# Kernel optimization log

Measured on AMD Instinct MI355X. Metric: run time of the kernel, lower is better.

## Reference

```python
import jax, jax.numpy as jnp
import numpy as np

B, S, HID = 1, 2048, 4096
NH, NKV, HD = 32, 8, 128
N_REP = NH // NKV
EPS = 1e-5
ROPE_THETA = 500000.0


def setup_inputs() -> dict:
    key = jax.random.key(0)
    ks = jax.random.split(key, 16)
    s = 0.02
    return {
        "hidden_states": jax.random.normal(ks[0], (B, S, HID), jnp.float32),
        "Wq": jax.random.normal(ks[1], (NH * HD, HID), jnp.float32) * s,
        "bq": jnp.zeros((NH * HD,), jnp.float32),
        "Wk": jax.random.normal(ks[2], (NKV * HD, HID), jnp.float32) * s,
        "bk": jnp.zeros((NKV * HD,), jnp.float32),
        "Wv": jax.random.normal(ks[3], (NKV * HD, HID), jnp.float32) * s,
        "bv": jnp.zeros((NKV * HD,), jnp.float32),
        "Wo": jax.random.normal(ks[4], (HID, HID), jnp.float32) * s,
        "bo": jnp.zeros((HID,), jnp.float32),
        "qn_g": jnp.ones((HD,), jnp.float32),
        "qn_b": jnp.zeros((HD,), jnp.float32),
        "kn_g": jnp.ones((HD,), jnp.float32),
        "kn_b": jnp.zeros((HD,), jnp.float32),
    }


def _layernorm(x, g, b):
    mu = jnp.mean(x, axis=-1, keepdims=True)
    var = jnp.var(x, axis=-1, keepdims=True)
    return (x - mu) * jax.lax.rsqrt(var + EPS) * g + b


def _rope_tables(seq_len, dtype):
    inv_freq = 1.0 / ROPE_THETA ** (jnp.arange(0, HD, 2, dtype=jnp.float32) / HD)
    pos = jnp.arange(seq_len, dtype=jnp.float32)
    freqs = pos[:, None] * inv_freq[None, :]          # (S, HD/2)
    emb = jnp.concatenate([freqs, freqs], axis=-1)    # (S, HD)
    return jnp.cos(emb).astype(dtype), jnp.sin(emb).astype(dtype)


def _rotate_half(x):
    x1, x2 = x[..., : HD // 2], x[..., HD // 2 :]
    return jnp.concatenate([-x2, x1], axis=-1)


def reference(hidden_states, Wq, bq, Wk, bk, Wv, bv, Wo, bo, qn_g, qn_b, kn_g, kn_b):
    x = hidden_states
    q = (x @ Wq.T + bq).reshape(B, S, NH, HD)
    k = (x @ Wk.T + bk).reshape(B, S, NKV, HD)
    v = (x @ Wv.T + bv).reshape(B, S, NKV, HD)
    # QK-Norm (LayerNorm over head_dim)
    q = _layernorm(q, qn_g, qn_b).transpose(0, 2, 1, 3)  # (B, NH, S, HD)
    k = _layernorm(k, kn_g, kn_b).transpose(0, 2, 1, 3)  # (B, NKV, S, HD)
    v = v.transpose(0, 2, 1, 3)
    # RoPE
    cos, sin = _rope_tables(S, x.dtype)  # (S, HD) each, broadcast over B, heads
    q = q * cos + _rotate_half(q) * sin
    k = k * cos + _rotate_half(k) * sin
    # GQA: repeat KV heads
    k = jnp.repeat(k, N_REP, axis=1)  # (B, NH, S, HD)
    v = jnp.repeat(v, N_REP, axis=1)
    # Causal attention
    scores = jnp.einsum("bhqd,bhkd->bhqk", q, k) / jnp.sqrt(jnp.float32(HD)).astype(x.dtype)
    causal = jnp.tril(jnp.ones((S, S), bool))
    scores = jnp.where(causal, scores, jnp.finfo(scores.dtype).min)
    attn = jax.nn.softmax(scores, axis=-1)
    out = jnp.einsum("bhqk,bhkd->bhqd", attn, v)
    out = out.transpose(0, 2, 1, 3).reshape(B, S, HID)
    return out @ Wo.T + bo
```

## Files before the change

kernel.cpp:

```cpp
#include <hip/hip_runtime.h>

typedef __bf16 bf16;
typedef __bf16 bf16x8 __attribute__((ext_vector_type(8)));
typedef __bf16 bf16x4 __attribute__((ext_vector_type(4)));
typedef float f32x4 __attribute__((ext_vector_type(4)));

#define S_LEN 2048
#define HID 4096
#define NH 32
#define NKV 8
#define HD 128
#define QSTR 6144
#define SCALE 0.08838834764831845f
#define QSCL 0.1275164918918885f
#define M2C 16.33f

template <int V> struct IC { static constexpr int value = V; };

__device__ __forceinline__ bf16x8 load8(const bf16* p) { return *(const bf16x8*)p; }
__device__ __forceinline__ bf16x8 load8(const float* p) {
    float4 a = *(const float4*)p;
    float4 b = *(const float4*)(p + 4);
    bf16x8 r;
    r[0] = (bf16)a.x; r[1] = (bf16)a.y; r[2] = (bf16)a.z; r[3] = (bf16)a.w;
    r[4] = (bf16)b.x; r[5] = (bf16)b.y; r[6] = (bf16)b.z; r[7] = (bf16)b.w;
    return r;
}

__device__ __forceinline__ void load_lds16(const bf16* g, bf16* l) {
    __builtin_amdgcn_global_load_lds(
        (const __attribute__((address_space(1))) void*)g,
        (__attribute__((address_space(3))) void*)l, 16, 0, 0);
}

template <int C> __device__ __forceinline__ void vmwait_if() {
    if constexpr (C >= 0) asm volatile("s_waitcnt vmcnt(%0)" ::"n"(C) : "memory");
}

__device__ __forceinline__ void lgkm0() {
    asm volatile("s_waitcnt lgkmcnt(0)" ::: "memory");
    __builtin_amdgcn_sched_barrier(0);
}

__global__ __launch_bounds__(256) void cvt5(const float* __restrict__ x,
                                            const float* __restrict__ Wq,
                                            const float* __restrict__ Wk,
                                            const float* __restrict__ Wv,
                                            const float* __restrict__ Wo,
                                            bf16* __restrict__ xb,
                                            bf16* __restrict__ Wqkv,
                                            bf16* __restrict__ Wob) {
    int i = blockIdx.x * 256 + threadIdx.x;
    const float* src;
    bf16* dst;
    if (i < 1048576)      { src = x  + (size_t)i * 8;              dst = xb + (size_t)i * 8; }
    else if (i < 3145728) { size_t j = i - 1048576; src = Wq + j * 8; dst = Wqkv + j * 8; }
    else if (i < 3670016) { size_t j = i - 3145728; src = Wk + j * 8; dst = Wqkv + 16777216 + j * 8; }
    else if (i < 4194304) { size_t j = i - 3670016; src = Wv + j * 8; dst = Wqkv + 20971520 + j * 8; }
    else                  { size_t j = i - 4194304; src = Wo + j * 8; dst = Wob + j * 8; }
    *(bf16x8*)dst = load8(src);
}

template <int BM, int BN, int WM, int WN, int BMODE, typename TO>
__global__ __launch_bounds__(512, 2) void gemm8(const bf16* __restrict__ A,
                                                const bf16* __restrict__ Bw,
                                                const float* __restrict__ b0,
                                                const float* __restrict__ b1,
                                                const float* __restrict__ b2,
                                                TO* __restrict__ out,
                                                int N, int K) {
    constexpr int RW  = BM / WM;
    constexpr int CW  = BN / WN;
    constexpr int FM  = RW / 16;
    constexpr int FN  = CW / 16;
    constexpr int FMH = FM / 2;
    constexpr int FNH0 = (FN + 1) / 2, FNH1 = FN - FNH0;
    constexpr int SZ0 = FNH0 * 16, SZ1 = FNH1 * 16;
    constexpr int AROWS_H = BM / 2;
    constexpr int B0ROWS = WN * SZ0, B1ROWS = WN * SZ1;
    constexpr int LA  = AROWS_H / 64;
    constexpr int LB0 = B0ROWS / 64, LB1 = B1ROWS / 64;
    constexpr int V0  = 2 * LA + LB0;
    constexpr int V3  = 2 * LA + LB0 + LB1;
    constexpr int V3T = LA + LB1;

    __shared__ __align__(16) bf16 AS[2 * BM * 64];
    __shared__ __align__(16) bf16 BS[2 * BN * 64];

    const int tid  = threadIdx.x;
    const int wave = tid >> 6;
    const int lane = tid & 63;
    const int quad = lane >> 4;
    const int l16  = lane & 15;
    const int wm   = wave / WN;
    const int wn   = wave % WN;

    const int gx   = gridDim.x;
    const int nwg  = gx * gridDim.y;
    const int orig = blockIdx.y * gx + blockIdx.x;
    int wg = orig;
    if ((nwg & 7) == 0) wg = (orig & 7) * (nwg >> 3) + (orig >> 3);
    const int row0 = (wg / gx) * BM;
    const int col0 = (wg % gx) * BN;

    auto stageA = [&](int mh, int bufv, int kt) {
#pragma unroll
        for (int j = 0; j < LA; ++j) {
            int c = j * 512 + tid;
            int r = c >> 3, pg = c & 7;
            int g = pg ^ (r & 7);
            int gr = (r / (RW / 2)) * RW + mh * (RW / 2) + (r % (RW / 2));
            load_lds16(&A[(size_t)(row0 + gr) * K + kt * 64 + g * 8],
                       &AS[bufv * (BM * 64) + mh * (AROWS_H * 64) + c * 8]);
        }
    };
    auto stageB0 = [&](int bufv, int kt) {
#pragma unroll
        for (int j = 0; j < LB0; ++j) {
            int c = j * 512 + tid;
            int r = c >> 3, pg = c & 7;
            int g = pg ^ (r & 7);
            int gc = (r / SZ0) * CW + (r % SZ0);
            load_lds16(&Bw[(size_t)(col0 + gc) * K + kt * 64 + g * 8],
                       &BS[bufv * (BN * 64) + c * 8]);
        }
    };
    auto stageB1 = [&](int bufv, int kt) {
#pragma unroll
        for (int j = 0; j < LB1; ++j) {
            int c = j * 512 + tid;
            int r = c >> 3, pg = c & 7;
            int g = pg ^ (r & 7);
            int gc = (r / SZ1) * CW + SZ0 + (r % SZ1);
            load_lds16(&Bw[(size_t)(col0 + gc) * K + kt * 64 + g * 8],
                       &BS[bufv * (BN * 64) + B0ROWS * 64 + c * 8]);
        }
    };

    f32x4 acc[FM][FN];
#pragma unroll
    for (int mi = 0; mi < FM; ++mi)
#pragma unroll
        for (int ni = 0; ni < FN; ++ni) { f32x4 z = {0.f, 0.f, 0.f, 0.f}; acc[mi][ni] = z; }

    bf16x8 af[FMH][2];
    bf16x8 bfv[FN][2];

    auto loadA = [&](int mh, int bufv) {
#pragma unroll
        for (int mi = 0; mi < FMH; ++mi)
#pragma unroll
            for (int ks = 0; ks < 2; ++ks) {
                int r = wm * (RW / 2) + mi * 16 + l16;
                int g = ks * 4 + quad;
                af[mi][ks] = *(const bf16x8*)&AS[bufv * (BM * 64) + mh * (AROWS_H * 64) +
                                                 r * 64 + ((g ^ (r & 7)) << 3)];
            }
    };
    auto loadB = [&](auto cNH, int bufv) {
        constexpr int NHv = decltype(cNH)::value;
        constexpr int CNT = NHv ? FNH1 : FNH0;
        constexpr int SZ  = NHv ? SZ1 : SZ0;
#pragma unroll
        for (int nj = 0; nj < CNT; ++nj)
#pragma unroll
            for (int ks = 0; ks < 2; ++ks) {
                int r = wn * SZ + nj * 16 + l16;
                int g = ks * 4 + quad;
                bfv[NHv * FNH0 + nj][ks] =
                    *(const bf16x8*)&BS[bufv * (BN * 64) + NHv * (B0ROWS * 64) +
                                        r * 64 + ((g ^ (r & 7)) << 3)];
            }
    };
    auto mmac = [&](auto cMH, auto cNH) {
        constexpr int MH = decltype(cMH)::value, NHv = decltype(cNH)::value;
        constexpr int NB = NHv ? FNH0 : 0, NE = NHv ? FN : FNH0;
        __builtin_amdgcn_s_setprio(1);
#pragma unroll
        for (int mi = 0; mi < FMH; ++mi)
#pragma unroll
            for (int ni = NB; ni < NE; ++ni)
#pragma unroll
                for (int ks = 0; ks < 2; ++ks)
                    acc[MH * FMH + mi][ni] = __builtin_amdgcn_mfma_f32_16x16x32_bf16(
                        af[mi][ks], bfv[ni][ks], acc[MH * FMH + mi][ni], 0, 0, 0);
        __builtin_amdgcn_s_setprio(0);
    };

    auto run_tile = [&](int t, auto cSA1, auto cSB1, auto cSA0, auto cSB0,
                        auto cV0, auto cV3) {
        const int buf = t & 1, nbuf = buf ^ 1;
        loadA(0, buf);
        loadB(IC<0>{}, buf);
        if constexpr (decltype(cSA1)::value) stageA(1, nbuf, t + 1);
        __builtin_amdgcn_s_barrier();
        lgkm0();
        mmac(IC<0>{}, IC<0>{});
        vmwait_if<decltype(cV0)::value>();
        __builtin_amdgcn_s_barrier();
        loadB(IC<1>{}, buf);
        if constexpr (decltype(cSB1)::value) stageB1(nbuf, t + 1);
        __builtin_amdgcn_s_barrier();
        lgkm0();
        mmac(IC<0>{}, IC<1>{});
        __builtin_amdgcn_s_barrier();
        loadA(1, buf);
        if constexpr (decltype(cSA0)::value) stageA(0, buf, t + 2);
        __builtin_amdgcn_s_barrier();
        lgkm0();
        mmac(IC<1>{}, IC<0>{});
        __builtin_amdgcn_s_barrier();
        if constexpr (decltype(cSB0)::value) stageB0(buf, t + 2);
        __builtin_amdgcn_s_barrier();
        lgkm0();
        mmac(IC<1>{}, IC<1>{});
        vmwait_if<decltype(cV3)::value>();
        __builtin_amdgcn_s_barrier();
    };

    stageA(0, 0, 0); stageB0(0, 0);
    stageA(1, 0, 0); stageB1(0, 0);
    stageA(0, 1, 1); stageB0(1, 1);
    vmwait_if<V3>();
    __builtin_amdgcn_s_barrier();

    const int NT = K >> 6;
    for (int t = 0; t < NT - 2; ++t)
        run_tile(t, IC<1>{}, IC<1>{}, IC<1>{}, IC<1>{}, IC<V0>{}, IC<V3>{});
    run_tile(NT - 2, IC<1>{}, IC<1>{}, IC<0>{}, IC<0>{}, IC<V0>{}, IC<V3T>{});
    run_tile(NT - 1, IC<0>{}, IC<0>{}, IC<0>{}, IC<0>{}, IC<0>{}, IC<-1>{});

#pragma unroll
    for (int ni = 0; ni < FN; ++ni) {
        int n = col0 + wn * CW + ni * 16 + l16;
        float bv;
        if (BMODE == 0) bv = b0[n];
        else bv = (n < 4096) ? b0[n] : ((n < 5120) ? b1[n - 4096] : b2[n - 5120]);
#pragma unroll
        for (int mi = 0; mi < FM; ++mi) {
            int m = row0 + wm * RW + mi * 16 + quad * 4;
#pragma unroll
            for (int reg = 0; reg < 4; ++reg)
                out[(size_t)(m + reg) * N + n] = (TO)(acc[mi][ni][reg] + bv);
        }
    }
}

__global__ __launch_bounds__(256) void ln_rope(bf16* __restrict__ qkv,
                                               const float* __restrict__ qg, const float* __restrict__ qbt,
                                               const float* __restrict__ kg, const float* __restrict__ kbt) {
    int row  = blockIdx.x * 4 + (threadIdx.x >> 6);
    int lane = threadIdx.x & 63;

    bf16* ptr;
    const float *g, *bb;
    int s;
    float osc;
    if (row < S_LEN * NH) {
        s   = row >> 5;
        ptr = qkv + (size_t)s * QSTR + (row & 31) * HD;
        g   = qg; bb = qbt; osc = QSCL;
    } else {
        int r2 = row - S_LEN * NH;
        s   = r2 >> 3;
        ptr = qkv + (size_t)s * QSTR + 4096 + (r2 & 7) * HD;
        g   = kg; bb = kbt; osc = 1.f;
    }

    float x1 = (float)ptr[lane];
    float x2 = (float)ptr[lane + 64];
    float sum = x1 + x2;
    float sq  = x1 * x1 + x2 * x2;
#pragma unroll
    for (int m = 1; m < 64; m <<= 1) {
        sum += __shfl_xor(sum, m);
        sq  += __shfl_xor(sq, m);
    }
    float mu  = sum * (1.f / 128.f);
    float var = sq * (1.f / 128.f) - mu * mu;
    float rs  = rsqrtf(var + 1e-5f);
    float n1  = (x1 - mu) * rs * g[lane] + bb[lane];
    float n2  = (x2 - mu) * rs * g[lane + 64] + bb[lane + 64];

    float inv = exp2f(-0.2958057514f * (float)lane);
    float ang = (float)s * inv;
    float sn, cs;
    sincosf(ang, &sn, &cs);

    ptr[lane]      = (bf16)((n1 * cs - n2 * sn) * osc);
    ptr[lane + 64] = (bf16)((n2 * cs + n1 * sn) * osc);
}

__global__ __launch_bounds__(256) void transpose_v(const bf16* __restrict__ qkv,
                                                   bf16* __restrict__ vT) {
    __shared__ bf16 Ts[64 * 64];
    const int c0 = blockIdx.x * 64;
    const int s0 = blockIdx.y * 64;
    const int tid = threadIdx.x;

#pragma unroll
    for (int i = 0; i < 2; ++i) {
        int cc = i * 256 + tid;
        int r = cc >> 3, col8 = cc & 7;
        *(bf16x8*)&Ts[r * 64 + ((col8 ^ (r & 7)) << 3)] =
            *(const bf16x8*)&qkv[(size_t)(s0 + r) * QSTR + 5120 + c0 + (col8 << 3)];
    }
    __syncthreads();
#pragma unroll
    for (int i = 0; i < 2; ++i) {
        int oc = i * 256 + tid;
        int c = oc & 63, sb = oc >> 6;
        bf16x8 r8;
#pragma unroll
        for (int j = 0; j < 8; ++j) {
            int sg = sb * 8 + j;
            r8[j] = Ts[sg * 64 + ((((c >> 3) ^ (sg & 7)) << 3) + (c & 7))];
        }
        *(bf16x8*)&vT[(size_t)(c0 + c) * S_LEN + s0 + sb * 8] = r8;
    }
}

__global__ __launch_bounds__(512) void attn6(const bf16* __restrict__ qkv,
                                             const bf16* __restrict__ vT,
                                             bf16* __restrict__ abuf) {
    const int pairp = blockIdx.x;
    const int kvh   = blockIdx.y;
    const int tid   = threadIdx.x;
    const int wave  = tid >> 6;
    const int lane  = tid & 63;
    const int quad  = lane >> 4;
    const int l16   = lane & 15;
    const int spw   = wave >> 2;
    const int hw    = wave & 3;
    const int h     = kvh * 4 + hw;

    __shared__ __align__(16) bf16 smem[4 * 8192 + 2 * 8192 + 8 * 2048];
    bf16* Ksb = smem;
    bf16* Vtb = smem + 4 * 8192;
    bf16* Psb = smem + 6 * 8192;

    bf16x8 onesf;
#pragma unroll
    for (int j = 0; j < 8; ++j) onesf[j] = (bf16)1.f;

    auto stageK = [&](int pr, int kb) {
#pragma unroll
        for (int j = 0; j < 4; ++j) {
            int c = j * 512 + tid;
            int tile = c >> 10, cc = c & 1023;
            int key = cc >> 4, pg = cc & 15;
            int g = pg ^ (key & 7);
            load_lds16(&qkv[(size_t)((2 * pr + tile) * 64 + key) * QSTR + 4096 +
                            kvh * HD + g * 8],
                       &Ksb[(kb * 2 + tile) * 8192 + cc * 8]);
        }
    };
    auto stageV = [&](int pr) {
#pragma unroll
        for (int j = 0; j < 4; ++j) {
            int c = j * 512 + tid;
            int tile = c >> 10, cc = c & 1023;
            int d = cc >> 3, pg = cc & 7;
            int g = pg ^ (d & 7);
            load_lds16(&vT[(size_t)(kvh * HD + d) * S_LEN + (2 * pr + tile) * 64 + g * 8],
                       &Vtb[tile * 8192 + cc * 8]);
        }
    };

    for (int ph = 0; ph < 2; ++ph) {
        const int qt  = ph ? (63 - pairp) : pairp;
        const int r0  = qt * 32;
        const int nkt = qt / 2 + 1;
        const int nit = (nkt + 1) >> 1;

        bf16x8 qf[2][4];
#pragma unroll
        for (int mi = 0; mi < 2; ++mi)
#pragma unroll
            for (int ks = 0; ks < 4; ++ks)
                qf[mi][ks] = *(const bf16x8*)&qkv[(size_t)(r0 + mi * 16 + l16) * QSTR +
                                                  h * HD + ks * 32 + quad * 8];

        f32x4 o_acc[2][8];
#pragma unroll
        for (int mi = 0; mi < 2; ++mi)
#pragma unroll
            for (int ni = 0; ni < 8; ++ni) {
                f32x4 z = {0.f, 0.f, 0.f, 0.f};
                o_acc[mi][ni] = z;
            }
        f32x4 lacc[2];
#pragma unroll
        for (int mi = 0; mi < 2; ++mi) { f32x4 z = {0.f, 0.f, 0.f, 0.f}; lacc[mi] = z; }

        stageK(0, 0);

        for (int it = 0; it < nit; ++it) {
            const int kb = it & 1;
            stageV(it);
            if (it + 1 < nit) { stageK(it + 1, kb ^ 1); vmwait_if<8>(); }
            else              { vmwait_if<4>(); }
            __syncthreads();

            const int kt = 2 * it + spw;
            const bf16* Kw = Ksb + (kb * 2 + spw) * 8192;
            const bf16* Vw = Vtb + spw * 8192;
            bf16* Pw = Psb + wave * 2048;

            if (kt < nkt) {
                f32x4 sacc[2][4];
#pragma unroll
                for (int mi = 0; mi < 2; ++mi)
#pragma unroll
                    for (int ni = 0; ni < 4; ++ni) {
                        f32x4 z = {0.f, 0.f, 0.f, 0.f};
                        sacc[mi][ni] = z;
                    }
                __builtin_amdgcn_s_setprio(1);
#pragma unroll
                for (int ks = 0; ks < 4; ++ks)
#pragma unroll
                    for (int ni = 0; ni < 4; ++ni) {
                        bf16x8 kf = *(const bf16x8*)&Kw[(ni * 16 + l16) * 128 +
                                                        ((((ks << 2) + quad) ^ (l16 & 7)) << 3)];
                        sacc[0][ni] = __builtin_amdgcn_mfma_f32_16x16x32_bf16(qf[0][ks], kf, sacc[0][ni], 0, 0, 0);
                        sacc[1][ni] = __builtin_amdgcn_mfma_f32_16x16x32_bf16(qf[1][ks], kf, sacc[1][ni], 0, 0, 0);
                    }
                __builtin_amdgcn_s_setprio(0);

#pragma unroll
                for (int mi = 0; mi < 2; ++mi)
#pragma unroll
                    for (int reg = 0; reg < 4; ++reg) {
                        int rloc = mi * 16 + quad * 4 + reg;
                        int qrow = r0 + rloc;
#pragma unroll
                        for (int ni = 0; ni < 4; ++ni) {
                            int key = kt * 64 + ni * 16 + l16;
                            float t = (key > qrow) ? -1e30f : (sacc[mi][ni][reg] - M2C);
                            float p = exp2f(t);
                            int blk = (ni * 2 + (l16 >> 3)) ^ (rloc & 7);
                            Pw[rloc * 64 + blk * 8 + (l16 & 7)] = (bf16)p;
                        }
                    }
            }

            if (it + 1 < nit) vmwait_if<4>();
            else              vmwait_if<0>();
            __syncthreads();

            if (kt < nkt) {
                const bf16* Vw2 = Vw;
                bf16* Pw2 = Pw;
                __builtin_amdgcn_s_setprio(1);
#pragma unroll
                for (int ks2 = 0; ks2 < 2; ++ks2) {
                    bf16x8 pa[2];
#pragma unroll
                    for (int mi = 0; mi < 2; ++mi) {
                        int rloc = mi * 16 + l16;
                        pa[mi] = *(const bf16x8*)&Pw2[rloc * 64 +
                                                      ((((ks2 << 2) + quad) ^ (rloc & 7)) << 3)];
                    }
#pragma unroll
                    for (int ni = 0; ni < 8; ++ni) {
                        int d = ni * 16 + l16;
                        bf16x8 vf = *(const bf16x8*)&Vw2[d * 64 + ((((ks2 << 2) + quad) ^ (d & 7)) << 3)];
                        o_acc[0][ni] = __builtin_amdgcn_mfma_f32_16x16x32_bf16(pa[0], vf, o_acc[0][ni], 0, 0, 0);
                        o_acc[1][ni] = __builtin_amdgcn_mfma_f32_16x16x32_bf16(pa[1], vf, o_acc[1][ni], 0, 0, 0);
                    }
                    lacc[0] = __builtin_amdgcn_mfma_f32_16x16x32_bf16(pa[0], onesf, lacc[0], 0, 0, 0);
                    lacc[1] = __builtin_amdgcn_mfma_f32_16x16x32_bf16(pa[1], onesf, lacc[1], 0, 0, 0);
                }
                __builtin_amdgcn_s_setprio(0);
            }
            __syncthreads();
        }

        float* M  = (float*)smem;
        float* Ls = (float*)&smem[4 * 8192];
        if (spw == 1) {
            float* Mw = M + hw * 4096;
#pragma unroll
            for (int mi = 0; mi < 2; ++mi)
#pragma unroll
                for (int ni = 0; ni < 8; ++ni)
#pragma unroll
                    for (int j = 0; j < 4; ++j)
                        Mw[((mi * 8 + ni) * 4 + j) * 64 + lane] = o_acc[mi][ni][j];
            if (l16 == 0)
#pragma unroll
                for (int mi = 0; mi < 2; ++mi)
#pragma unroll
                    for (int reg = 0; reg < 4; ++reg)
                        Ls[hw * 32 + mi * 16 + quad * 4 + reg] = lacc[mi][reg];
        }
        __syncthreads();
        if (spw == 0) {
            float* Mw = M + hw * 4096;
#pragma unroll
            for (int mi = 0; mi < 2; ++mi) {
                float linv[4];
#pragma unroll
                for (int reg = 0; reg < 4; ++reg)
                    linv[reg] = 1.f / fmaxf(lacc[mi][reg] +
                                            Ls[hw * 32 + mi * 16 + quad * 4 + reg], 1e-30f);
#pragma unroll
                for (int ni = 0; ni < 8; ++ni)
#pragma unroll
                    for (int reg = 0; reg < 4; ++reg) {
                        float v = o_acc[mi][ni][reg] + Mw[((mi * 8 + ni) * 4 + reg) * 64 + lane];
                        int s = r0 + mi * 16 + quad * 4 + reg;
                        abuf[(size_t)s * HID + h * HD + ni * 16 + l16] = (bf16)(v * linv[reg]);
                    }
            }
        }
        __syncthreads();
    }
}

template <typename TA, typename TO>
__global__ __launch_bounds__(256) void gemm_bt(const TA* __restrict__ A,
                                               const float* __restrict__ W,
                                               const float* __restrict__ bias,
                                               TO* __restrict__ out,
                                               int N, int K) {
    __shared__ __align__(16) bf16 As[128 * 64];
    __shared__ __align__(16) bf16 Bs[128 * 64];
    const int tid = threadIdx.x, wave = tid >> 6, lane = tid & 63;
    const int quad = lane >> 4, l16 = lane & 15, wm = wave >> 1, wn = wave & 1;
    const int row0 = blockIdx.y * 128, col0 = blockIdx.x * 128;
    f32x4 acc[4][4];
#pragma unroll
    for (int mi = 0; mi < 4; ++mi)
#pragma unroll
        for (int ni = 0; ni < 4; ++ni) { f32x4 z = {0.f,0.f,0.f,0.f}; acc[mi][ni] = z; }
    for (int k0 = 0; k0 < K; k0 += 64) {
#pragma unroll
        for (int i = 0; i < 4; ++i) {
            int c = i * 256 + tid, r = c >> 3, col8 = (c & 7) << 3;
            *(bf16x8*)&As[r * 64 + col8] = load8(&A[(size_t)(row0 + r) * K + k0 + col8]);
            *(bf16x8*)&Bs[r * 64 + col8] = load8(&W[(size_t)(col0 + r) * K + k0 + col8]);
        }
        __syncthreads();
#pragma unroll
        for (int ks = 0; ks < 2; ++ks) {
            bf16x8 af[4], bfr[4];
#pragma unroll
            for (int mi = 0; mi < 4; ++mi)
                af[mi] = *(const bf16x8*)&As[(wm * 64 + mi * 16 + l16) * 64 + ks * 32 + quad * 8];
#pragma unroll
            for (int ni = 0; ni < 4; ++ni)
                bfr[ni] = *(const bf16x8*)&Bs[(wn * 64 + ni * 16 + l16) * 64 + ks * 32 + quad * 8];
#pragma unroll
            for (int mi = 0; mi < 4; ++mi)
#pragma unroll
                for (int ni = 0; ni < 4; ++ni)
                    acc[mi][ni] = __builtin_amdgcn_mfma_f32_16x16x32_bf16(af[mi], bfr[ni], acc[mi][ni], 0, 0, 0);
        }
        __syncthreads();
    }
#pragma unroll
    for (int ni = 0; ni < 4; ++ni) {
        int n = col0 + wn * 64 + ni * 16 + l16;
        float bv = bias[n];
#pragma unroll
        for (int mi = 0; mi < 4; ++mi) {
            int m = row0 + wm * 64 + mi * 16 + quad * 4;
#pragma unroll
            for (int reg = 0; reg < 4; ++reg)
                out[(size_t)(m + reg) * N + n] = (TO)(acc[mi][ni][reg] + bv);
        }
    }
}

__global__ __launch_bounds__(256) void ln_rope_f(bf16* __restrict__ qb, bf16* __restrict__ kb,
                                                 const float* __restrict__ qg, const float* __restrict__ qbt,
                                                 const float* __restrict__ kg, const float* __restrict__ kbt) {
    int row = blockIdx.x * 4 + (threadIdx.x >> 6);
    int lane = threadIdx.x & 63;
    bf16* ptr; const float *g, *bb; int s;
    if (row < S_LEN * NH) { s = row >> 5; ptr = qb + (size_t)s * (NH * HD) + (row & 31) * HD; g = qg; bb = qbt; }
    else { int r2 = row - S_LEN * NH; s = r2 >> 3; ptr = kb + (size_t)s * (NKV * HD) + (r2 & 7) * HD; g = kg; bb = kbt; }
    float x1 = (float)ptr[lane], x2 = (float)ptr[lane + 64];
    float sum = x1 + x2, sq = x1 * x1 + x2 * x2;
#pragma unroll
    for (int m = 1; m < 64; m <<= 1) { sum += __shfl_xor(sum, m); sq += __shfl_xor(sq, m); }
    float mu = sum * (1.f / 128.f), var = sq * (1.f / 128.f) - mu * mu;
    float rs = rsqrtf(var + 1e-5f);
    float n1 = (x1 - mu) * rs * g[lane] + bb[lane];
    float n2 = (x2 - mu) * rs * g[lane + 64] + bb[lane + 64];
    float inv = powf(500000.f, -(float)lane * (1.f / 64.f));
    float ang = (float)s * inv, sn, cs;
    sincosf(ang, &sn, &cs);
    ptr[lane] = (bf16)(n1 * cs - n2 * sn);
    ptr[lane + 64] = (bf16)(n2 * cs + n1 * sn);
}

__global__ __launch_bounds__(256) void attn_old(const bf16* __restrict__ qbuf,
                                                const bf16* __restrict__ kbuf,
                                                const bf16* __restrict__ vbuf,
                                                bf16* __restrict__ obuf) {
    const int qi = blockIdx.x, hh = blockIdx.y, kvh = hh >> 2;
    __shared__ __align__(16) bf16 Qs[64 * 128];
    __shared__ __align__(16) bf16 Ks2[64 * 128];
    __shared__ __align__(16) bf16 Vt2[128 * 80];
    __shared__ __align__(16) float Ss[64 * 64];
    __shared__ __align__(16) bf16 Ps2[64 * 64];
    __shared__ float mS[64], lS[64], aS[64];
    const int tid = threadIdx.x, wave = tid >> 6, lane = tid & 63;
    const int quad = lane >> 4, l16 = lane & 15;
#pragma unroll
    for (int i = 0; i < 4; ++i) {
        int c = i * 256 + tid, r = c >> 4, col8 = (c & 15) << 3;
        *(int4*)&Qs[r * 128 + col8] = *(const int4*)&qbuf[(size_t)(qi * 64 + r) * HID + hh * HD + col8];
    }
    if (tid < 64) { mS[tid] = -1e30f; lS[tid] = 0.f; }
    f32x4 o_acc[8];
#pragma unroll
    for (int i = 0; i < 8; ++i) { f32x4 z = {0.f,0.f,0.f,0.f}; o_acc[i] = z; }
    __syncthreads();
    for (int kt = 0; kt <= qi; ++kt) {
#pragma unroll
        for (int i = 0; i < 4; ++i) {
            int c = i * 256 + tid, r = c >> 4, col8 = (c & 15) << 3;
            const size_t gofs = (size_t)(kt * 64 + r) * (NKV * HD) + kvh * HD + col8;
            *(int4*)&Ks2[r * 128 + col8] = *(const int4*)&kbuf[gofs];
            bf16x8 vv = *(const bf16x8*)&vbuf[gofs];
#pragma unroll
            for (int e = 0; e < 8; ++e) Vt2[(col8 + e) * 80 + r] = vv[e];
        }
        __syncthreads();
        f32x4 sacc[4];
#pragma unroll
        for (int ni = 0; ni < 4; ++ni) { f32x4 z = {0.f,0.f,0.f,0.f}; sacc[ni] = z; }
#pragma unroll
        for (int ks = 0; ks < 4; ++ks) {
            bf16x8 a = *(const bf16x8*)&Qs[(wave * 16 + l16) * 128 + ks * 32 + quad * 8];
#pragma unroll
            for (int ni = 0; ni < 4; ++ni) {
                bf16x8 b = *(const bf16x8*)&Ks2[(ni * 16 + l16) * 128 + ks * 32 + quad * 8];
                sacc[ni] = __builtin_amdgcn_mfma_f32_16x16x32_bf16(a, b, sacc[ni], 0, 0, 0);
            }
        }
#pragma unroll
        for (int ni = 0; ni < 4; ++ni)
#pragma unroll
            for (int reg = 0; reg < 4; ++reg) {
                int r = wave * 16 + quad * 4 + reg, cc = ni * 16 + l16;
                float sv = sacc[ni][reg] * SCALE;
                if (kt * 64 + cc > qi * 64 + r) sv = -1e30f;
                Ss[r * 64 + cc] = sv;
            }
        __syncthreads();
        {
            int r = tid >> 2, j = tid & 3;
            float vals[16], mloc = -1e30f;
#pragma unroll
            for (int c = 0; c < 16; ++c) { vals[c] = Ss[r * 64 + j * 16 + c]; mloc = fmaxf(mloc, vals[c]); }
            mloc = fmaxf(mloc, __shfl_xor(mloc, 1));
            mloc = fmaxf(mloc, __shfl_xor(mloc, 2));
            float mold = mS[r], mnew = fmaxf(mold, mloc), ssum = 0.f;
#pragma unroll
            for (int c = 0; c < 16; ++c) {
                float p = __expf(vals[c] - mnew);
                ssum += p;
                Ps2[r * 64 + j * 16 + c] = (bf16)p;
            }
            ssum += __shfl_xor(ssum, 1);
            ssum += __shfl_xor(ssum, 2);
            if (j == 0) { float alpha = __expf(mold - mnew); mS[r] = mnew; lS[r] = lS[r] * alpha + ssum; aS[r] = alpha; }
        }
        __syncthreads();
        {
            float al2[4];
#pragma unroll
            for (int reg = 0; reg < 4; ++reg) al2[reg] = aS[wave * 16 + quad * 4 + reg];
#pragma unroll
            for (int ni = 0; ni < 8; ++ni)
#pragma unroll
                for (int reg = 0; reg < 4; ++reg) o_acc[ni][reg] *= al2[reg];
#pragma unroll
            for (int ks = 0; ks < 2; ++ks) {
                bf16x8 a = *(const bf16x8*)&Ps2[(wave * 16 + l16) * 64 + ks * 32 + quad * 8];
#pragma unroll
                for (int ni = 0; ni < 8; ++ni) {
                    bf16x8 b = *(const bf16x8*)&Vt2[(ni * 16 + l16) * 80 + ks * 32 + quad * 8];
                    o_acc[ni] = __builtin_amdgcn_mfma_f32_16x16x32_bf16(a, b, o_acc[ni], 0, 0, 0);
                }
            }
        }
        __syncthreads();
    }
    {
        float linv[4];
#pragma unroll
        for (int reg = 0; reg < 4; ++reg) linv[reg] = 1.f / fmaxf(lS[wave * 16 + quad * 4 + reg], 1e-20f);
#pragma unroll
        for (int ni = 0; ni < 8; ++ni)
#pragma unroll
            for (int reg = 0; reg < 4; ++reg) {
                int r = wave * 16 + quad * 4 + reg;
                obuf[(size_t)(qi * 64 + r) * HID + hh * HD + ni * 16 + l16] = (bf16)(o_acc[ni][reg] * linv[reg]);
            }
    }
}

extern "C" void kernel_launch(void* const* d_in, const int* in_sizes, int n_in,
                              void* d_out, int out_size, void* d_ws, size_t ws_size,
                              hipStream_t stream) {
    const float* x   = (const float*)d_in[0];
    const float* Wq  = (const float*)d_in[1];
    const float* bq  = (const float*)d_in[2];
    const float* Wk  = (const float*)d_in[3];
    const float* bk  = (const float*)d_in[4];
    const float* Wv  = (const float*)d_in[5];
    const float* bv  = (const float*)d_in[6];
    const float* Wo  = (const float*)d_in[7];
    const float* bo  = (const float*)d_in[8];
    const float* qg  = (const float*)d_in[9];
    const float* qbt = (const float*)d_in[10];
    const float* kg  = (const float*)d_in[11];
    const float* kbt = (const float*)d_in[12];
    float* out = (float*)d_out;

    const size_t NEED = 130547712;
    if (ws_size >= NEED) {
        char* p = (char*)d_ws;
        bf16*  xb   = (bf16*)p;
        bf16*  Wqkv = (bf16*)(p + 16777216);
        bf16*  abuf = (bf16*)p;
        bf16*  Wob  = (bf16*)(p + 67108864);
        bf16*  qkv  = (bf16*)(p + 100663296);
        bf16*  vT   = (bf16*)(p + 125829120);

        cvt5<<<24576, 256, 0, stream>>>(x, Wq, Wk, Wv, Wo, xb, Wqkv, Wob);

        gemm8<256, 192, 2, 4, 1, bf16><<<dim3(32, 8), 512, 0, stream>>>(
            xb, Wqkv, bq, bk, bv, qkv, QSTR, 4096);

        ln_rope<<<dim3((S_LEN * (NH + NKV)) / 4), 256, 0, stream>>>(qkv, qg, qbt, kg, kbt);

        transpose_v<<<dim3(16, 32), 256, 0, stream>>>(qkv, vT);

        attn6<<<dim3(32, 8), 512, 0, stream>>>(qkv, vT, abuf);

        gemm8<256, 128, 4, 2, 0, float><<<dim3(32, 8), 512, 0, stream>>>(
            abuf, Wob, bo, bo, bo, out, 4096, 4096);
    } else {
        char* ws = (char*)d_ws;
        bf16* qbuf = (bf16*)(ws);
        bf16* kbuf = (bf16*)(ws + (16u << 20));
        bf16* vbuf = (bf16*)(ws + (20u << 20));
        bf16* abuf = (bf16*)(ws + (24u << 20));
        gemm_bt<float, bf16><<<dim3(32, 16), 256, 0, stream>>>(x, Wq, bq, qbuf, 4096, 4096);
        gemm_bt<float, bf16><<<dim3(8, 16), 256, 0, stream>>>(x, Wk, bk, kbuf, 1024, 4096);
        gemm_bt<float, bf16><<<dim3(8, 16), 256, 0, stream>>>(x, Wv, bv, vbuf, 1024, 4096);
        ln_rope_f<<<dim3((S_LEN * (NH + NKV)) / 4), 256, 0, stream>>>(qbuf, kbuf, qg, qbt, kg, kbt);
        attn_old<<<dim3(32, 32), 256, 0, stream>>>(qbuf, kbuf, vbuf, abuf);
        gemm_bt<bf16, float><<<dim3(32, 16), 256, 0, stream>>>(abuf, Wo, bo, out, 4096, 4096);
    }
}
```

Measured before the change: 512.6 us.

## Merge LN-RoPE and V-transpose into one kernel and remap GEMM tile order per XCD

The separate ln_rope and transpose_v launches are combined into one prep kernel. Its first 5120 blocks each process 16 rows of LayerNorm+RoPE, and the remaining 512 blocks transpose V, which removes one launch and gives each block more rows to amortize. For the 32x8 GEMM grids, the workgroup-to-tile mapping now gives each XCD a contiguous 4x8 patch of output tiles, which should improve L2 reuse of A and B. The attention kernel loses two redundant pointer aliases.

```diff
diff --git a/kernel.cpp b/kernel.cpp
--- a/kernel.cpp
+++ b/kernel.cpp
@@ -96,12 +96,21 @@
     const int wn   = wave % WN;
 
     const int gx   = gridDim.x;
-    const int nwg  = gx * gridDim.y;
     const int orig = blockIdx.y * gx + blockIdx.x;
-    int wg = orig;
-    if ((nwg & 7) == 0) wg = (orig & 7) * (nwg >> 3) + (orig >> 3);
-    const int row0 = (wg / gx) * BM;
-    const int col0 = (wg % gx) * BN;
+    int row_p, col_p;
+    if (gx == 32 && gridDim.y == 8) {
+        int xcd = orig & 7, idx = orig >> 3;
+        row_p = ((xcd >> 2) << 2) + (idx >> 3);
+        col_p = ((xcd & 3) << 3) + (idx & 7);
+    } else {
+        int nwg = gx * gridDim.y;
+        int wg = orig;
+        if ((nwg & 7) == 0) wg = (orig & 7) * (nwg >> 3) + (orig >> 3);
+        row_p = wg / gx;
+        col_p = wg % gx;
+    }
+    const int row0 = row_p * BM;
+    const int col0 = col_p * BN;
 
     auto stageA = [&](int mh, int bufv, int kt) {
 #pragma unroll
@@ -246,77 +255,82 @@
     }
 }
 
-__global__ __launch_bounds__(256) void ln_rope(bf16* __restrict__ qkv,
-                                               const float* __restrict__ qg, const float* __restrict__ qbt,
-                                               const float* __restrict__ kg, const float* __restrict__ kbt) {
-    int row  = blockIdx.x * 4 + (threadIdx.x >> 6);
-    int lane = threadIdx.x & 63;
-
-    bf16* ptr;
-    const float *g, *bb;
-    int s;
-    float osc;
-    if (row < S_LEN * NH) {
-        s   = row >> 5;
-        ptr = qkv + (size_t)s * QSTR + (row & 31) * HD;
-        g   = qg; bb = qbt; osc = QSCL;
+__global__ __launch_bounds__(256) void prep(bf16* __restrict__ qkv,
+                                            bf16* __restrict__ vT,
+                                            const float* __restrict__ qg, const float* __restrict__ qbt,
+                                            const float* __restrict__ kg, const float* __restrict__ kbt) {
+    __shared__ bf16 Ts[64 * 64];
+    const int b   = blockIdx.x;
+    const int tid = threadIdx.x;
+
+    if (b < 5120) {
+        int lane = tid & 63;
+#pragma unroll
+        for (int rr = 0; rr < 4; ++rr) {
+            int row = b * 16 + rr * 4 + (tid >> 6);
+            bf16* ptr;
+            const float *g, *bb;
+            int s;
+            float osc;
+            if (row < S_LEN * NH) {
+                s   = row >> 5;
+                ptr = qkv + (size_t)s * QSTR + (row & 31) * HD;
+                g   = qg; bb = qbt; osc = QSCL;
+            } else {
+                int r2 = row - S_LEN * NH;
+                s   = r2 >> 3;
+                ptr = qkv + (size_t)s * QSTR + 4096 + (r2 & 7) * HD;
+                g   = kg; bb = kbt; osc = 1.f;
+            }
+
+            float x1 = (float)ptr[lane];
+            float x2 = (float)ptr[lane + 64];
+            float sum = x1 + x2;
+            float sq  = x1 * x1 + x2 * x2;
+#pragma unroll
+            for (int m = 1; m < 64; m <<= 1) {
+                sum += __shfl_xor(sum, m);
+                sq  += __shfl_xor(sq, m);
+            }
+            float mu  = sum * (1.f / 128.f);
+            float var = sq * (1.f / 128.f) - mu * mu;
+            float rs  = rsqrtf(var + 1e-5f);
+            float n1  = (x1 - mu) * rs * g[lane] + bb[lane];
+            float n2  = (x2 - mu) * rs * g[lane + 64] + bb[lane + 64];
+
+            float inv = exp2f(-0.2958057514f * (float)lane);
+            float ang = (float)s * inv;
+            float sn, cs;
+            sincosf(ang, &sn, &cs);
+
+            ptr[lane]      = (bf16)((n1 * cs - n2 * sn) * osc);
+            ptr[lane + 64] = (bf16)((n2 * cs + n1 * sn) * osc);
+        }
     } else {
-        int r2 = row - S_LEN * NH;
-        s   = r2 >> 3;
-        ptr = qkv + (size_t)s * QSTR + 4096 + (r2 & 7) * HD;
-        g   = kg; bb = kbt; osc = 1.f;
-    }
-
-    float x1 = (float)ptr[lane];
-    float x2 = (float)ptr[lane + 64];
-    float sum = x1 + x2;
-    float sq  = x1 * x1 + x2 * x2;
-#pragma unroll
-    for (int m = 1; m < 64; m <<= 1) {
-        sum += __shfl_xor(sum, m);
-        sq  += __shfl_xor(sq, m);
-    }
-    float mu  = sum * (1.f / 128.f);
-    float var = sq * (1.f / 128.f) - mu * mu;
-    float rs  = rsqrtf(var + 1e-5f);
-    float n1  = (x1 - mu) * rs * g[lane] + bb[lane];
-    float n2  = (x2 - mu) * rs * g[lane + 64] + bb[lane + 64];
-
-    float inv = exp2f(-0.2958057514f * (float)lane);
-    float ang = (float)s * inv;
-    float sn, cs;
-    sincosf(ang, &sn, &cs);
-
-    ptr[lane]      = (bf16)((n1 * cs - n2 * sn) * osc);
-    ptr[lane + 64] = (bf16)((n2 * cs + n1 * sn) * osc);
-}
-
-__global__ __launch_bounds__(256) void transpose_v(const bf16* __restrict__ qkv,
-                                                   bf16* __restrict__ vT) {
-    __shared__ bf16 Ts[64 * 64];
-    const int c0 = blockIdx.x * 64;
-    const int s0 = blockIdx.y * 64;
-    const int tid = threadIdx.x;
-
-#pragma unroll
-    for (int i = 0; i < 2; ++i) {
-        int cc = i * 256 + tid;
-        int r = cc >> 3, col8 = cc & 7;
-        *(bf16x8*)&Ts[r * 64 + ((col8 ^ (r & 7)) << 3)] =
-            *(const bf16x8*)&qkv[(size_t)(s0 + r) * QSTR + 5120 + c0 + (col8 << 3)];
-    }
-    __syncthreads();
-#pragma unroll
-    for (int i = 0; i < 2; ++i) {
-        int oc = i * 256 + tid;
-        int c = oc & 63, sb = oc >> 6;
-        bf16x8 r8;
-#pragma unroll
-        for (int j = 0; j < 8; ++j) {
-            int sg = sb * 8 + j;
-            r8[j] = Ts[sg * 64 + ((((c >> 3) ^ (sg & 7)) << 3) + (c & 7))];
-        }
-        *(bf16x8*)&vT[(size_t)(c0 + c) * S_LEN + s0 + sb * 8] = r8;
+        const int t  = b - 5120;
+        const int c0 = (t & 15) * 64;
+        const int s0 = (t >> 4) * 64;
+
+#pragma unroll
+        for (int i = 0; i < 2; ++i) {
+            int cc = i * 256 + tid;
+            int r = cc >> 3, col8 = cc & 7;
+            *(bf16x8*)&Ts[r * 64 + ((col8 ^ (r & 7)) << 3)] =
+                *(const bf16x8*)&qkv[(size_t)(s0 + r) * QSTR + 5120 + c0 + (col8 << 3)];
+        }
+        __syncthreads();
+#pragma unroll
+        for (int i = 0; i < 2; ++i) {
+            int oc = i * 256 + tid;
+            int c = oc & 63, sb = oc >> 6;
+            bf16x8 r8;
+#pragma unroll
+            for (int j = 0; j < 8; ++j) {
+                int sg = sb * 8 + j;
+                r8[j] = Ts[sg * 64 + ((((c >> 3) ^ (sg & 7)) << 3) + (c & 7))];
+            }
+            *(bf16x8*)&vT[(size_t)(c0 + c) * S_LEN + s0 + sb * 8] = r8;
+        }
     }
 }
 
@@ -450,8 +464,6 @@
             __syncthreads();
 
             if (kt < nkt) {
-                const bf16* Vw2 = Vw;
-                bf16* Pw2 = Pw;
                 __builtin_amdgcn_s_setprio(1);
 #pragma unroll
                 for (int ks2 = 0; ks2 < 2; ++ks2) {
@@ -459,13 +471,13 @@
 #pragma unroll
                     for (int mi = 0; mi < 2; ++mi) {
                         int rloc = mi * 16 + l16;
-                        pa[mi] = *(const bf16x8*)&Pw2[rloc * 64 +
-                                                      ((((ks2 << 2) + quad) ^ (rloc & 7)) << 3)];
+                        pa[mi] = *(const bf16x8*)&Pw[rloc * 64 +
+                                                     ((((ks2 << 2) + quad) ^ (rloc & 7)) << 3)];
                     }
 #pragma unroll
                     for (int ni = 0; ni < 8; ++ni) {
                         int d = ni * 16 + l16;
-                        bf16x8 vf = *(const bf16x8*)&Vw2[d * 64 + ((((ks2 << 2) + quad) ^ (d & 7)) << 3)];
+                        bf16x8 vf = *(const bf16x8*)&Vw[d * 64 + ((((ks2 << 2) + quad) ^ (d & 7)) << 3)];
                         o_acc[0][ni] = __builtin_amdgcn_mfma_f32_16x16x32_bf16(pa[0], vf, o_acc[0][ni], 0, 0, 0);
                         o_acc[1][ni] = __builtin_amdgcn_mfma_f32_16x16x32_bf16(pa[1], vf, o_acc[1][ni], 0, 0, 0);
                     }
@@ -739,9 +751,7 @@
         gemm8<256, 192, 2, 4, 1, bf16><<<dim3(32, 8), 512, 0, stream>>>(
             xb, Wqkv, bq, bk, bv, qkv, QSTR, 4096);
 
-        ln_rope<<<dim3((S_LEN * (NH + NKV)) / 4), 256, 0, stream>>>(qkv, qg, qbt, kg, kbt);
-
-        transpose_v<<<dim3(16, 32), 256, 0, stream>>>(qkv, vT);
+        prep<<<5632, 256, 0, stream>>>(qkv, vT, qg, qbt, kg, kbt);
 
         attn6<<<dim3(32, 8), 512, 0, stream>>>(qkv, vT, abuf);
 
```

Result: faster. 501.6 us (-2.1%).
